# Kernel optimization log

Measured on AMD Instinct MI355X. Metric: run time of the kernel, lower is better.

## Reference

```python
import jax, jax.numpy as jnp
import numpy as np

NUM_USERS = 100000
NUM_ITEMS = 100000
D = 64          # embed_dim
B = 4096        # batch of users (rows of sparse interaction matrix)
NNZ = 204800    # nonzeros in sparse user-item matrix (~50 items/user)
N = 1048576     # number of (user,item) pairs to score
DROPOUT = 0.2


def setup_inputs() -> dict:
    key = jax.random.key(0)
    ks = jax.random.split(key, 10)
    return {
        "user_ids": jax.random.randint(ks[0], (B,), 0, NUM_USERS, dtype=jnp.int32),
        "bat_idx": jax.random.randint(ks[1], (N,), 0, B, dtype=jnp.int32),
        "sp_row": jax.random.randint(ks[2], (NNZ,), 0, B, dtype=jnp.int32),
        "sp_col": jax.random.randint(ks[3], (NNZ,), 0, NUM_ITEMS, dtype=jnp.int32),
        "bat_items": jax.random.randint(ks[4], (N,), 0, NUM_ITEMS, dtype=jnp.int32),
        # learned parameters (normal init for embeddings, zeros for offset/bias, as in reset_parameters)
        "en_emb": jax.random.normal(ks[5], (NUM_ITEMS, D), dtype=jnp.float32) * 0.01,
        "en_offset": jnp.zeros((D,), dtype=jnp.float32),
        "de_emb": jax.random.normal(ks[6], (NUM_ITEMS, D), dtype=jnp.float32) * 0.01,
        "de_bias": jnp.zeros((NUM_ITEMS,), dtype=jnp.float32),
        "user_emb": jax.random.normal(ks[7], (NUM_USERS, D), dtype=jnp.float32) * 0.01,
    }


def reference(user_ids, bat_idx, sp_row, sp_col, bat_items,
              en_emb, en_offset, de_emb, de_bias, user_emb):
    keep = 1.0 - DROPOUT
    # dropout_sparse: bernoulli keep-mask on sparse nnz values (binary 1.0), rescaled by 1/keep
    drop_mask = jax.random.bernoulli(jax.random.key(42), keep, (NNZ,))
    vals = drop_mask.astype(en_emb.dtype) / keep  # corrupted sparse values [NNZ]

    # sparse @ dense: sum_j A[b,j] * en_emb[j]  ->  gather + segment_sum  -> [B, D]
    hidden = jax.ops.segment_sum(vals[:, None] * en_emb[sp_col], sp_row, num_segments=B)
    hidden = jnp.tanh(hidden + user_emb[user_ids] + en_offset[None, :])

    # decode: inner product of gathered hidden rows and item embeddings
    h = hidden[bat_idx]                      # [N, D]
    de_i = de_emb[bat_items]                 # [N, D]
    ratings = jnp.sum(h * de_i, axis=-1) + de_bias[bat_items]  # [N]

    # l2 reg over unique bat_items rows (mask-based == torch.unique gather)
    item_mask = jnp.zeros((NUM_ITEMS,), en_emb.dtype).at[bat_items].set(1.0)
    reg_loss = 0.5 * (
        jnp.sum(item_mask * jnp.sum(en_emb ** 2, axis=-1))
        + jnp.sum(en_offset ** 2)
        + jnp.sum(user_emb[user_ids] ** 2)
        + jnp.sum(item_mask * jnp.sum(de_emb ** 2, axis=-1))
        + jnp.sum(item_mask * de_bias ** 2)
    )
    return ratings, reg_loss
```

## Files before the change

### kernel.cpp

```cpp
#include <hip/hip_runtime.h>
#include <hip/hip_bf16.h>

#define PARTITIONABLE 1
#define NB 8
#define CAPB 136192
#define FATB 2048
#define CAPR 128
#define RSB 200
#define SCVT 1024
#define HBLK 1024
#define REGF 64
#define REGB_FB 256

__device__ __forceinline__ unsigned rotl32(unsigned x, int r) {
    return (x << r) | (x >> (32 - r));
}

__device__ __forceinline__ void threefry2x32(unsigned k0, unsigned k1,
                                             unsigned& x0, unsigned& x1) {
    unsigned ks0 = k0, ks1 = k1, ks2 = k0 ^ k1 ^ 0x1BD11BDAu;
    x0 += ks0; x1 += ks1;
#define TF_R(r) { x0 += x1; x1 = rotl32(x1, r); x1 ^= x0; }
    TF_R(13) TF_R(15) TF_R(26) TF_R(6)   x0 += ks1; x1 += ks2 + 1u;
    TF_R(17) TF_R(29) TF_R(16) TF_R(24)  x0 += ks2; x1 += ks0 + 2u;
    TF_R(13) TF_R(15) TF_R(26) TF_R(6)   x0 += ks0; x1 += ks1 + 3u;
    TF_R(17) TF_R(29) TF_R(16) TF_R(24)  x0 += ks1; x1 += ks2 + 4u;
    TF_R(13) TF_R(15) TF_R(26) TF_R(6)   x0 += ks2; x1 += ks0 + 5u;
#undef TF_R
}

__device__ __forceinline__ bool keep_mask(int i, int nnz) {
#if PARTITIONABLE
    unsigned x0 = 0u, x1 = (unsigned)i;
    threefry2x32(0u, 42u, x0, x1);
    unsigned bits = x0 ^ x1;
#else
    int half = nnz >> 1;
    int j = (i < half) ? i : i - half;
    unsigned x0 = (unsigned)j, x1 = (unsigned)(j + half);
    threefry2x32(0u, 42u, x0, x1);
    unsigned bits = (i < half) ? x0 : x1;
#endif
    float u = __uint_as_float((bits >> 9) | 0x3f800000u) - 1.0f;
    return u < 0.8f;
}

__device__ __forceinline__ unsigned short f2bf(float f) {
    unsigned u = __float_as_uint(f);
    return (unsigned short)((u + 0x7FFFu + ((u >> 16) & 1u)) >> 16);
}

__device__ __forceinline__ float bfdot8(uint4 h, uint4 d) {
    float s;
    s  = __uint_as_float(h.x << 16)         * __uint_as_float(d.x << 16);
    s += __uint_as_float(h.x & 0xFFFF0000u) * __uint_as_float(d.x & 0xFFFF0000u);
    s += __uint_as_float(h.y << 16)         * __uint_as_float(d.y << 16);
    s += __uint_as_float(h.y & 0xFFFF0000u) * __uint_as_float(d.y & 0xFFFF0000u);
    s += __uint_as_float(h.z << 16)         * __uint_as_float(d.z << 16);
    s += __uint_as_float(h.z & 0xFFFF0000u) * __uint_as_float(d.z & 0xFFFF0000u);
    s += __uint_as_float(h.w << 16)         * __uint_as_float(d.w << 16);
    s += __uint_as_float(h.w & 0xFFFF0000u) * __uint_as_float(d.w & 0xFFFF0000u);
    return s;
}

__global__ void k_prep(const int* __restrict__ bat_idx, const int* __restrict__ bat_items,
                       unsigned char* __restrict__ mask, int* __restrict__ cursor,
                       unsigned* __restrict__ perm, unsigned* __restrict__ inv,
                       const int* __restrict__ sp_row, const int* __restrict__ sp_col,
                       int* __restrict__ rowcur, unsigned* __restrict__ srow,
                       const float* __restrict__ en_emb, const float* __restrict__ de_emb,
                       const float* __restrict__ de_bias, const float* __restrict__ user_emb,
                       const int* __restrict__ user_ids, const float* __restrict__ en_off,
                       unsigned short* __restrict__ debf, float* __restrict__ sq,
                       float* __restrict__ reg_ws,
                       int N, int num_items, int nnz, int B) {
    __shared__ int sh[4096];
    if (blockIdx.x < 256) {
        if (threadIdx.x < NB) sh[threadIdx.x] = 0;
        __syncthreads();
        const int per = N / 256;
        const int base_n = blockIdx.x * per;
        const int iters = per / blockDim.x;
        unsigned packed[16];
        int bkt[16];
        for (int it = 0; it < iters; ++it) {
            int n = base_n + it * blockDim.x + threadIdx.x;
            int item = bat_items[n];
            int bidx = bat_idx[n];
            mask[item] = 1;
            int b = (int)(((unsigned long long)(unsigned)item * NB) / (unsigned)num_items);
            packed[it] = ((unsigned)item << 12) | (unsigned)bidx;
            bkt[it] = b;
            atomicAdd(&sh[b], 1);
        }
        __syncthreads();
        if (threadIdx.x < NB) {
            int c = sh[threadIdx.x];
            sh[threadIdx.x] = atomicAdd(&cursor[threadIdx.x], c);
        }
        __syncthreads();
        for (int it = 0; it < iters; ++it) {
            int n = base_n + it * blockDim.x + threadIdx.x;
            int pos = atomicAdd(&sh[bkt[it]], 1);
            unsigned gpos = (unsigned)bkt[it] * CAPB + (unsigned)min(pos, CAPB - 1);
            perm[gpos] = packed[it];
            inv[n] = gpos;
        }
    } else if (blockIdx.x < 256 + RSB) {
        const int blk = blockIdx.x - 256;
        for (int i = threadIdx.x; i < B; i += blockDim.x) sh[i] = 0;
        __syncthreads();
        const int per = nnz / RSB;
        const int base = blk * per;
        const int iters = per / blockDim.x;
        unsigned pk[8];
        int rw[8];
        for (int it = 0; it < iters; ++it) {
            int i = base + it * blockDim.x + threadIdx.x;
            int row = sp_row[i];
            int col = sp_col[i];
            bool k = keep_mask(i, nnz);
            pk[it] = (unsigned)col;
            rw[it] = k ? row : -1;
            if (k) atomicAdd(&sh[row], 1);
        }
        __syncthreads();
        for (int i = threadIdx.x; i < B; i += blockDim.x) {
            int c = sh[i];
            if (c) sh[i] = atomicAdd(&rowcur[i], c);
        }
        __syncthreads();
        for (int it = 0; it < iters; ++it) {
            if (rw[it] >= 0) {
                int pos = atomicAdd(&sh[rw[it]], 1);
                srow[(size_t)rw[it] * CAPR + min(pos, CAPR - 1)] = pk[it];
            }
        }
    } else {
        const int bx = blockIdx.x - (256 + RSB);
        const int stride = SCVT * blockDim.x;
        for (int t = bx * blockDim.x + threadIdx.x; t < num_items * 16; t += stride) {
            int i = t >> 4, l = t & 15;
            float4 d = *reinterpret_cast<const float4*>(de_emb + (size_t)i * 64 + l * 4);
            float4 e = *reinterpret_cast<const float4*>(en_emb + (size_t)i * 64 + l * 4);
            ushort4 o;
            o.x = f2bf(d.x); o.y = f2bf(d.y); o.z = f2bf(d.z); o.w = f2bf(d.w);
            reinterpret_cast<ushort4*>(debf)[t] = o;
            float q = e.x*e.x + e.y*e.y + e.z*e.z + e.w*e.w
                    + d.x*d.x + d.y*d.y + d.z*d.z + d.w*d.w;
            if (l == 0) { float bb = de_bias[i]; q += bb * bb; }
            q += __shfl_xor(q, 1);
            q += __shfl_xor(q, 2);
            q += __shfl_xor(q, 4);
            q += __shfl_xor(q, 8);
            if (l == 0) sq[i] = q;
        }
        float s = 0.f;
        for (int t = bx * blockDim.x + threadIdx.x; t < B * 16; t += stride) {
            int b = t >> 4, l = t & 15;
            int uid = user_ids[b];
            float4 u = *reinterpret_cast<const float4*>(user_emb + (size_t)uid * 64 + l * 4);
            s += u.x*u.x + u.y*u.y + u.z*u.z + u.w*u.w;
        }
        if (bx == 0 && threadIdx.x < 64) {
            float o = en_off[threadIdx.x];
            s += o * o;
        }
        for (int m = 1; m < 64; m <<= 1) s += __shfl_xor(s, m);
        float* wsum = (float*)sh;
        if ((threadIdx.x & 63) == 0) wsum[threadIdx.x >> 6] = s;
        __syncthreads();
        if (threadIdx.x == 0)
            atomicAdd(reg_ws, wsum[0] + wsum[1] + wsum[2] + wsum[3]);
    }
}

__global__ void k_hidden_reg(const unsigned* __restrict__ srow, const int* __restrict__ rowcur,
                             const float* __restrict__ en_emb, const float* __restrict__ user_emb,
                             const int* __restrict__ user_ids, const float* __restrict__ en_off,
                             unsigned short* __restrict__ hb,
                             const unsigned char* __restrict__ mask,
                             const float* __restrict__ sq,
                             float* __restrict__ reg_ws, int B, int num_items) {
    if (blockIdx.x < HBLK) {
        const int lane = threadIdx.x & 63;
        const int row = (blockIdx.x * blockDim.x + threadIdx.x) >> 6;
        if (row >= B) return;
        const int cnt = min(rowcur[row], CAPR);
        const unsigned* sr = srow + (size_t)row * CAPR;
        float acc0 = 0.f, acc1 = 0.f, acc2 = 0.f, acc3 = 0.f;
        float acc4 = 0.f, acc5 = 0.f, acc6 = 0.f, acc7 = 0.f;
        for (int j0 = 0; j0 < cnt; j0 += 64) {
            unsigned ev = (j0 + lane < cnt) ? sr[j0 + lane] : 0u;
            int m = min(64, cnt - j0);
            int jj = 0;
            for (; jj + 7 < m; jj += 8) {
                unsigned e0 = __shfl(ev, jj);
                unsigned e1 = __shfl(ev, jj + 1);
                unsigned e2 = __shfl(ev, jj + 2);
                unsigned e3 = __shfl(ev, jj + 3);
                unsigned e4 = __shfl(ev, jj + 4);
                unsigned e5 = __shfl(ev, jj + 5);
                unsigned e6 = __shfl(ev, jj + 6);
                unsigned e7 = __shfl(ev, jj + 7);
                acc0 += en_emb[(size_t)e0 * 64 + lane];
                acc1 += en_emb[(size_t)e1 * 64 + lane];
                acc2 += en_emb[(size_t)e2 * 64 + lane];
                acc3 += en_emb[(size_t)e3 * 64 + lane];
                acc4 += en_emb[(size_t)e4 * 64 + lane];
                acc5 += en_emb[(size_t)e5 * 64 + lane];
                acc6 += en_emb[(size_t)e6 * 64 + lane];
                acc7 += en_emb[(size_t)e7 * 64 + lane];
            }
            for (; jj + 3 < m; jj += 4) {
                unsigned e0 = __shfl(ev, jj);
                unsigned e1 = __shfl(ev, jj + 1);
                unsigned e2 = __shfl(ev, jj + 2);
                unsigned e3 = __shfl(ev, jj + 3);
                acc0 += en_emb[(size_t)e0 * 64 + lane];
                acc1 += en_emb[(size_t)e1 * 64 + lane];
                acc2 += en_emb[(size_t)e2 * 64 + lane];
                acc3 += en_emb[(size_t)e3 * 64 + lane];
            }
            for (; jj < m; ++jj) {
                unsigned e0 = __shfl(ev, jj);
                acc0 += en_emb[(size_t)e0 * 64 + lane];
            }
        }
        int uid = user_ids[row];
        float hval = 1.25f * (((acc0 + acc1) + (acc2 + acc3))
                            + ((acc4 + acc5) + (acc6 + acc7)))
                   + user_emb[(size_t)uid * 64 + lane] + en_off[lane];
        hb[(size_t)row * 64 + lane] = f2bf(tanhf(hval));
    } else {
        const int bx = blockIdx.x - HBLK;
        const int stride = REGF * blockDim.x;
        float s = 0.f;
        for (int i = bx * blockDim.x + threadIdx.x; i < num_items; i += stride)
            s += (float)mask[i] * sq[i];
        for (int m = 1; m < 64; m <<= 1) s += __shfl_xor(s, m);
        __shared__ float wsum[4];
        if ((threadIdx.x & 63) == 0) wsum[threadIdx.x >> 6] = s;
        __syncthreads();
        if (threadIdx.x == 0)
            atomicAdd(reg_ws, wsum[0] + wsum[1] + wsum[2] + wsum[3]);
    }
}

__global__ void k_ratings_bkt(const unsigned short* __restrict__ hb,
                              const unsigned short* __restrict__ debf,
                              const float* __restrict__ de_bias,
                              const unsigned* __restrict__ perm, const int* __restrict__ cursor,
                              float* __restrict__ r_perm) {
    const int bkt = blockIdx.x & (NB - 1);
    const int cnt = cursor[bkt];
    const int l = threadIdx.x & 7;
    const int gid = (blockIdx.x >> 3) * (blockDim.x >> 3) + (threadIdx.x >> 3);
    const int gpb = (gridDim.x >> 3) * (blockDim.x >> 3);
    const unsigned* pb = perm + (size_t)bkt * CAPB;
    float* rb = r_perm + (size_t)bkt * CAPB;

    int slot = gid;
    for (; slot + 3 * gpb < cnt; slot += 4 * gpb) {
        unsigned p0 = pb[slot];
        unsigned p1 = pb[slot + gpb];
        unsigned p2 = pb[slot + 2 * gpb];
        unsigned p3 = pb[slot + 3 * gpb];
        int it0 = (int)(p0 >> 12), b0 = (int)(p0 & 0xFFFu);
        int it1 = (int)(p1 >> 12), b1 = (int)(p1 & 0xFFFu);
        int it2 = (int)(p2 >> 12), b2 = (int)(p2 & 0xFFFu);
        int it3 = (int)(p3 >> 12), b3 = (int)(p3 & 0xFFFu);
        uint4 h0 = *reinterpret_cast<const uint4*>(hb   + (size_t)b0  * 64 + l * 8);
        uint4 d0 = *reinterpret_cast<const uint4*>(debf + (size_t)it0 * 64 + l * 8);
        uint4 h1 = *reinterpret_cast<const uint4*>(hb   + (size_t)b1  * 64 + l * 8);
        uint4 d1 = *reinterpret_cast<const uint4*>(debf + (size_t)it1 * 64 + l * 8);
        uint4 h2 = *reinterpret_cast<const uint4*>(hb   + (size_t)b2  * 64 + l * 8);
        uint4 d2 = *reinterpret_cast<const uint4*>(debf + (size_t)it2 * 64 + l * 8);
        uint4 h3 = *reinterpret_cast<const uint4*>(hb   + (size_t)b3  * 64 + l * 8);
        uint4 d3 = *reinterpret_cast<const uint4*>(debf + (size_t)it3 * 64 + l * 8);
        float s0 = bfdot8(h0, d0);
        float s1 = bfdot8(h1, d1);
        float s2 = bfdot8(h2, d2);
        float s3 = bfdot8(h3, d3);
        s0 += __shfl_xor(s0, 1); s1 += __shfl_xor(s1, 1);
        s2 += __shfl_xor(s2, 1); s3 += __shfl_xor(s3, 1);
        s0 += __shfl_xor(s0, 2); s1 += __shfl_xor(s1, 2);
        s2 += __shfl_xor(s2, 2); s3 += __shfl_xor(s3, 2);
        s0 += __shfl_xor(s0, 4); s1 += __shfl_xor(s1, 4);
        s2 += __shfl_xor(s2, 4); s3 += __shfl_xor(s3, 4);
        if (l == 0) {
            rb[slot]           = s0 + de_bias[it0];
            rb[slot + gpb]     = s1 + de_bias[it1];
            rb[slot + 2 * gpb] = s2 + de_bias[it2];
            rb[slot + 3 * gpb] = s3 + de_bias[it3];
        }
    }
    for (; slot < cnt; slot += gpb) {
        unsigned p = pb[slot];
        int item = (int)(p >> 12), bidx = (int)(p & 0xFFFu);
        uint4 hv = *reinterpret_cast<const uint4*>(hb   + (size_t)bidx * 64 + l * 8);
        uint4 dv = *reinterpret_cast<const uint4*>(debf + (size_t)item * 64 + l * 8);
        float s = bfdot8(hv, dv);
        s += __shfl_xor(s, 1);
        s += __shfl_xor(s, 2);
        s += __shfl_xor(s, 4);
        if (l == 0) rb[slot] = s + de_bias[item];
    }
}

__global__ void k_unperm(const unsigned* __restrict__ inv, const float* __restrict__ r_perm,
                         const float* __restrict__ reg_ws, float* __restrict__ out, int N) {
    const int quads = N >> 2;
    const int stride = gridDim.x * blockDim.x;
    for (int q = blockIdx.x * blockDim.x + threadIdx.x; q < quads; q += stride) {
        uint4 iv = reinterpret_cast<const uint4*>(inv)[q];
        float4 o;
        o.x = r_perm[iv.x];
        o.y = r_perm[iv.y];
        o.z = r_perm[iv.z];
        o.w = r_perm[iv.w];
        reinterpret_cast<float4*>(out)[q] = o;
    }
    if (blockIdx.x == 0 && threadIdx.x == 0)
        out[N] = 0.5f * reg_ws[0];
}

__global__ void k_mask(const int* __restrict__ bat_items, unsigned char* __restrict__ mask,
                       int N) {
    int t = blockIdx.x * blockDim.x + threadIdx.x;
    if (t < N) mask[bat_items[t]] = 1;
}

__global__ void k_ratings(const float* __restrict__ hidden, const float* __restrict__ de_emb,
                          const float* __restrict__ de_bias,
                          const int* __restrict__ bat_idx, const int* __restrict__ bat_items,
                          float* __restrict__ out, int N) {
    const int l = threadIdx.x & 15;
    const int gid = (blockIdx.x * blockDim.x + threadIdx.x) >> 4;
    const int gstride = (gridDim.x * blockDim.x) >> 4;
    for (int n = gid; n < N; n += gstride) {
        int b  = bat_idx[n];
        int it = bat_items[n];
        float4 hv = *reinterpret_cast<const float4*>(hidden + (size_t)b  * 64 + l * 4);
        float4 dv = *reinterpret_cast<const float4*>(de_emb + (size_t)it * 64 + l * 4);
        float s = hv.x*dv.x + hv.y*dv.y + hv.z*dv.z + hv.w*dv.w;
        s += __shfl_xor(s, 1);
        s += __shfl_xor(s, 2);
        s += __shfl_xor(s, 4);
        s += __shfl_xor(s, 8);
        if (l == 0) out[n] = s + de_bias[it];
    }
}

__global__ void k_scatter(const int* __restrict__ sp_row, const int* __restrict__ sp_col,
                          const float* __restrict__ en_emb, float* __restrict__ hidden,
                          int nnz) {
    const int lane = threadIdx.x & 63;
    const int wave = (blockIdx.x * blockDim.x + threadIdx.x) >> 6;
    const int nwaves = (gridDim.x * blockDim.x) >> 6;
    for (int i = wave; i < nnz; i += nwaves) {
        if (!keep_mask(i, nnz)) continue;
        int row = sp_row[i];
        int col = sp_col[i];
        float v = 1.25f * en_emb[(size_t)col * 64 + lane];
        atomicAdd(&hidden[row * 64 + lane], v);
    }
}

__global__ void k_hfinish(float* __restrict__ hidden, const float* __restrict__ user_emb,
                          const int* __restrict__ user_ids, const float* __restrict__ en_off,
                          int B) {
    int t = blockIdx.x * blockDim.x + threadIdx.x;
    if (t >= B * 64) return;
    int b = t >> 6, d = t & 63;
    int uid = user_ids[b];
    float h = hidden[t] + user_emb[(size_t)uid * 64 + d] + en_off[d];
    hidden[t] = tanhf(h);
}

__global__ void k_reg_fb(const unsigned char* __restrict__ mask,
                         const float* __restrict__ en_emb, const float* __restrict__ de_emb,
                         const float* __restrict__ de_bias,
                         const float* __restrict__ user_emb, const int* __restrict__ user_ids,
                         const float* __restrict__ en_off,
                         float* __restrict__ reg, int num_items, int B) {
    const int stride = gridDim.x * blockDim.x;
    float s = 0.f;
    for (int t = blockIdx.x * blockDim.x + threadIdx.x; t < num_items * 16; t += stride) {
        int i = t >> 4, l = t & 15;
        if (mask[i]) {
            float4 e = *reinterpret_cast<const float4*>(en_emb + (size_t)i * 64 + l * 4);
            float4 d = *reinterpret_cast<const float4*>(de_emb + (size_t)i * 64 + l * 4);
            s += e.x*e.x + e.y*e.y + e.z*e.z + e.w*e.w
               + d.x*d.x + d.y*d.y + d.z*d.z + d.w*d.w;
            if (l == 0) { float bb = de_bias[i]; s += bb * bb; }
        }
    }
    for (int t = blockIdx.x * blockDim.x + threadIdx.x; t < B * 16; t += stride) {
        int b = t >> 4, l = t & 15;
        int uid = user_ids[b];
        float4 u = *reinterpret_cast<const float4*>(user_emb + (size_t)uid * 64 + l * 4);
        s += u.x*u.x + u.y*u.y + u.z*u.z + u.w*u.w;
    }
    if (blockIdx.x == 0 && threadIdx.x < 64) {
        float o = en_off[threadIdx.x];
        s += o * o;
    }
    for (int m = 1; m < 64; m <<= 1) s += __shfl_xor(s, m);
    __shared__ float wsum[4];
    if ((threadIdx.x & 63) == 0) wsum[threadIdx.x >> 6] = s;
    __syncthreads();
    if (threadIdx.x == 0)
        atomicAdd(reg, 0.5f * (wsum[0] + wsum[1] + wsum[2] + wsum[3]));
}

extern "C" void kernel_launch(void* const* d_in, const int* in_sizes, int n_in,
                              void* d_out, int out_size, void* d_ws, size_t ws_size,
                              hipStream_t stream) {
    const int*   user_ids  = (const int*)  d_in[0];
    const int*   bat_idx   = (const int*)  d_in[1];
    const int*   sp_row    = (const int*)  d_in[2];
    const int*   sp_col    = (const int*)  d_in[3];
    const int*   bat_items = (const int*)  d_in[4];
    const float* en_emb    = (const float*)d_in[5];
    const float* en_off    = (const float*)d_in[6];
    const float* de_emb    = (const float*)d_in[7];
    const float* de_bias   = (const float*)d_in[8];
    const float* user_emb  = (const float*)d_in[9];

    const int B         = in_sizes[0];
    const int N         = in_sizes[1];
    const int NNZ       = in_sizes[2];
    const int NUM_ITEMS = in_sizes[8];

    float* out = (float*)d_out;

    char* ws = (char*)d_ws;
    size_t off = 0;
    unsigned char* mask = (unsigned char*)(ws + off);
    off += ((size_t)NUM_ITEMS + 255) & ~(size_t)255;
    int* cursor = (int*)(ws + off);               off += 256;
    int* rowcur = (int*)(ws + off);               off += (size_t)B * 4;
    float* reg_ws = (float*)(ws + off);           off += 256;
    const size_t zero_bytes = off;
    float* hidden = (float*)(ws + off);           off += (size_t)B * 64 * 4;
    unsigned* perm   = (unsigned*)(ws + off);     off += (size_t)NB * CAPB * 4;
    unsigned* inv    = (unsigned*)(ws + off);     off += (size_t)N * 4;
    float*    r_perm = (float*)(ws + off);
    unsigned* srow   = (unsigned*)r_perm;
    size_t tail = (size_t)NB * CAPB * 4;
    if ((size_t)B * CAPR * 4 > tail) tail = (size_t)B * CAPR * 4;
    off += tail;
    unsigned short* hb   = (unsigned short*)(ws + off);  off += (size_t)B * 64 * 2;
    off = (off + 15) & ~(size_t)15;
    unsigned short* debf = (unsigned short*)(ws + off);  off += (size_t)NUM_ITEMS * 64 * 2;
    float* sq = (float*)(ws + off);                      off += (size_t)NUM_ITEMS * 4;

    const bool sorted_path =
        (ws_size >= off) && (N == (1 << 20)) && (B == 4096) &&
        (NUM_ITEMS <= (1 << 17)) && (NUM_ITEMS >= 65536) &&
        (NUM_ITEMS % 4 == 0) &&
        (NNZ % (RSB * 256) == 0) && (NNZ / RSB <= CAPR * 256);

    hipMemsetAsync(ws, 0, zero_bytes, stream);

    if (sorted_path) {
        k_prep<<<256 + RSB + SCVT, 256, 0, stream>>>(
            bat_idx, bat_items, mask, cursor, perm, inv,
            sp_row, sp_col, rowcur, srow,
            en_emb, de_emb, de_bias, user_emb, user_ids, en_off,
            debf, sq, reg_ws, N, NUM_ITEMS, NNZ, B);
        k_hidden_reg<<<HBLK + REGF, 256, 0, stream>>>(
            srow, rowcur, en_emb, user_emb, user_ids, en_off, hb,
            mask, sq, reg_ws, B, NUM_ITEMS);
        k_ratings_bkt<<<FATB, 256, 0, stream>>>(hb, debf, de_bias, perm, cursor, r_perm);
        k_unperm<<<1024, 256, 0, stream>>>(inv, r_perm, reg_ws, out, N);
    } else {
        hipMemsetAsync(hidden, 0, (size_t)B * 64 * 4, stream);
        hipMemsetAsync(out + N, 0, sizeof(float), stream);
        k_mask<<<(N + 255) / 256, 256, 0, stream>>>(bat_items, mask, N);
        k_scatter<<<FATB, 256, 0, stream>>>(sp_row, sp_col, en_emb, hidden, NNZ);
        k_hfinish<<<(B * 64 + 255) / 256, 256, 0, stream>>>(hidden, user_emb, user_ids,
                                                            en_off, B);
        k_ratings<<<FATB, 256, 0, stream>>>(hidden, de_emb, de_bias, bat_idx, bat_items, out, N);
        k_reg_fb<<<REGB_FB, 256, 0, stream>>>(mask, en_emb, de_emb, de_bias,
                                              user_emb, user_ids, en_off, out + N, NUM_ITEMS, B);
    }
}
```

Measured before the change: 178.8 us.

## Store original index alongside bucketed pair and scatter ratings directly, drop unpermute kernel

Each bucketed (item,batch) entry now carries its original output index as a uint2, so the ratings kernel writes each result straight to out[n] instead of to a permuted buffer. The separate unpermute kernel and the inv/r_perm arrays are removed, and the reg_loss write moves into the ratings kernel. This saves one launch and the gather pass, at the cost of doubling the perm read bytes and making the output stores scattered rather than coalesced.

```diff
diff --git a/kernel.cpp b/kernel.cpp
--- a/kernel.cpp
+++ b/kernel.cpp
@@ -65,7 +65,7 @@
 
 __global__ void k_prep(const int* __restrict__ bat_idx, const int* __restrict__ bat_items,
                        unsigned char* __restrict__ mask, int* __restrict__ cursor,
-                       unsigned* __restrict__ perm, unsigned* __restrict__ inv,
+                       uint2* __restrict__ perm2,
                        const int* __restrict__ sp_row, const int* __restrict__ sp_col,
                        int* __restrict__ rowcur, unsigned* __restrict__ srow,
                        const float* __restrict__ en_emb, const float* __restrict__ de_emb,
@@ -103,8 +103,7 @@
             int n = base_n + it * blockDim.x + threadIdx.x;
             int pos = atomicAdd(&sh[bkt[it]], 1);
             unsigned gpos = (unsigned)bkt[it] * CAPB + (unsigned)min(pos, CAPB - 1);
-            perm[gpos] = packed[it];
-            inv[n] = gpos;
+            perm2[gpos] = make_uint2(packed[it], (unsigned)n);
         }
     } else if (blockIdx.x < 256 + RSB) {
         const int blk = blockIdx.x - 256;
@@ -250,26 +249,28 @@
 __global__ void k_ratings_bkt(const unsigned short* __restrict__ hb,
                               const unsigned short* __restrict__ debf,
                               const float* __restrict__ de_bias,
-                              const unsigned* __restrict__ perm, const int* __restrict__ cursor,
-                              float* __restrict__ r_perm) {
+                              const uint2* __restrict__ perm2, const int* __restrict__ cursor,
+                              const float* __restrict__ reg_ws,
+                              float* __restrict__ out, int N) {
+    if (blockIdx.x == 0 && threadIdx.x == 0)
+        out[N] = 0.5f * reg_ws[0];
     const int bkt = blockIdx.x & (NB - 1);
     const int cnt = cursor[bkt];
     const int l = threadIdx.x & 7;
     const int gid = (blockIdx.x >> 3) * (blockDim.x >> 3) + (threadIdx.x >> 3);
     const int gpb = (gridDim.x >> 3) * (blockDim.x >> 3);
-    const unsigned* pb = perm + (size_t)bkt * CAPB;
-    float* rb = r_perm + (size_t)bkt * CAPB;
+    const uint2* pb = perm2 + (size_t)bkt * CAPB;
 
     int slot = gid;
     for (; slot + 3 * gpb < cnt; slot += 4 * gpb) {
-        unsigned p0 = pb[slot];
-        unsigned p1 = pb[slot + gpb];
-        unsigned p2 = pb[slot + 2 * gpb];
-        unsigned p3 = pb[slot + 3 * gpb];
-        int it0 = (int)(p0 >> 12), b0 = (int)(p0 & 0xFFFu);
-        int it1 = (int)(p1 >> 12), b1 = (int)(p1 & 0xFFFu);
-        int it2 = (int)(p2 >> 12), b2 = (int)(p2 & 0xFFFu);
-        int it3 = (int)(p3 >> 12), b3 = (int)(p3 & 0xFFFu);
+        uint2 p0 = pb[slot];
+        uint2 p1 = pb[slot + gpb];
+        uint2 p2 = pb[slot + 2 * gpb];
+        uint2 p3 = pb[slot + 3 * gpb];
+        int it0 = (int)(p0.x >> 12), b0 = (int)(p0.x & 0xFFFu);
+        int it1 = (int)(p1.x >> 12), b1 = (int)(p1.x & 0xFFFu);
+        int it2 = (int)(p2.x >> 12), b2 = (int)(p2.x & 0xFFFu);
+        int it3 = (int)(p3.x >> 12), b3 = (int)(p3.x & 0xFFFu);
         uint4 h0 = *reinterpret_cast<const uint4*>(hb   + (size_t)b0  * 64 + l * 8);
         uint4 d0 = *reinterpret_cast<const uint4*>(debf + (size_t)it0 * 64 + l * 8);
         uint4 h1 = *reinterpret_cast<const uint4*>(hb   + (size_t)b1  * 64 + l * 8);
@@ -289,40 +290,23 @@
         s0 += __shfl_xor(s0, 4); s1 += __shfl_xor(s1, 4);
         s2 += __shfl_xor(s2, 4); s3 += __shfl_xor(s3, 4);
         if (l == 0) {
-            rb[slot]           = s0 + de_bias[it0];
-            rb[slot + gpb]     = s1 + de_bias[it1];
-            rb[slot + 2 * gpb] = s2 + de_bias[it2];
-            rb[slot + 3 * gpb] = s3 + de_bias[it3];
+            out[p0.y] = s0 + de_bias[it0];
+            out[p1.y] = s1 + de_bias[it1];
+            out[p2.y] = s2 + de_bias[it2];
+            out[p3.y] = s3 + de_bias[it3];
         }
     }
     for (; slot < cnt; slot += gpb) {
-        unsigned p = pb[slot];
-        int item = (int)(p >> 12), bidx = (int)(p & 0xFFFu);
+        uint2 p = pb[slot];
+        int item = (int)(p.x >> 12), bidx = (int)(p.x & 0xFFFu);
         uint4 hv = *reinterpret_cast<const uint4*>(hb   + (size_t)bidx * 64 + l * 8);
         uint4 dv = *reinterpret_cast<const uint4*>(debf + (size_t)item * 64 + l * 8);
         float s = bfdot8(hv, dv);
         s += __shfl_xor(s, 1);
         s += __shfl_xor(s, 2);
         s += __shfl_xor(s, 4);
-        if (l == 0) rb[slot] = s + de_bias[item];
-    }
-}
-
-__global__ void k_unperm(const unsigned* __restrict__ inv, const float* __restrict__ r_perm,
-                         const float* __restrict__ reg_ws, float* __restrict__ out, int N) {
-    const int quads = N >> 2;
-    const int stride = gridDim.x * blockDim.x;
-    for (int q = blockIdx.x * blockDim.x + threadIdx.x; q < quads; q += stride) {
-        uint4 iv = reinterpret_cast<const uint4*>(inv)[q];
-        float4 o;
-        o.x = r_perm[iv.x];
-        o.y = r_perm[iv.y];
-        o.z = r_perm[iv.z];
-        o.w = r_perm[iv.w];
-        reinterpret_cast<float4*>(out)[q] = o;
-    }
-    if (blockIdx.x == 0 && threadIdx.x == 0)
-        out[N] = 0.5f * reg_ws[0];
+        if (l == 0) out[p.y] = s + de_bias[item];
+    }
 }
 
 __global__ void k_mask(const int* __restrict__ bat_items, unsigned char* __restrict__ mask,
@@ -444,13 +428,9 @@
     float* reg_ws = (float*)(ws + off);           off += 256;
     const size_t zero_bytes = off;
     float* hidden = (float*)(ws + off);           off += (size_t)B * 64 * 4;
-    unsigned* perm   = (unsigned*)(ws + off);     off += (size_t)NB * CAPB * 4;
-    unsigned* inv    = (unsigned*)(ws + off);     off += (size_t)N * 4;
-    float*    r_perm = (float*)(ws + off);
-    unsigned* srow   = (unsigned*)r_perm;
-    size_t tail = (size_t)NB * CAPB * 4;
-    if ((size_t)B * CAPR * 4 > tail) tail = (size_t)B * CAPR * 4;
-    off += tail;
+    off = (off + 15) & ~(size_t)15;
+    uint2* perm2 = (uint2*)(ws + off);            off += (size_t)NB * CAPB * 8;
+    unsigned* srow = (unsigned*)(ws + off);       off += (size_t)B * CAPR * 4;
     unsigned short* hb   = (unsigned short*)(ws + off);  off += (size_t)B * 64 * 2;
     off = (off + 15) & ~(size_t)15;
     unsigned short* debf = (unsigned short*)(ws + off);  off += (size_t)NUM_ITEMS * 64 * 2;
@@ -466,15 +446,15 @@
 
     if (sorted_path) {
         k_prep<<<256 + RSB + SCVT, 256, 0, stream>>>(
-            bat_idx, bat_items, mask, cursor, perm, inv,
+            bat_idx, bat_items, mask, cursor, perm2,
             sp_row, sp_col, rowcur, srow,
             en_emb, de_emb, de_bias, user_emb, user_ids, en_off,
             debf, sq, reg_ws, N, NUM_ITEMS, NNZ, B);
         k_hidden_reg<<<HBLK + REGF, 256, 0, stream>>>(
             srow, rowcur, en_emb, user_emb, user_ids, en_off, hb,
             mask, sq, reg_ws, B, NUM_ITEMS);
-        k_ratings_bkt<<<FATB, 256, 0, stream>>>(hb, debf, de_bias, perm, cursor, r_perm);
-        k_unperm<<<1024, 256, 0, stream>>>(inv, r_perm, reg_ws, out, N);
+        k_ratings_bkt<<<FATB, 256, 0, stream>>>(hb, debf, de_bias, perm2, cursor,
+                                                reg_ws, out, N);
     } else {
         hipMemsetAsync(hidden, 0, (size_t)B * 64 * 4, stream);
         hipMemsetAsync(out + N, 0, sizeof(float), stream);
```

After: 175.5 us (median of 2 runs). No clear change (-1.8%).
